# Optimization experiments

Hardware: AMD Instinct MI355X
Metric: run time of the kernel (lower is better)

The kernel has to match this reference:

```python
import jax, jax.numpy as jnp
import numpy as np

B, N, K, F_IN, F_OUT = 8, 2048, 32, 256, 256


def setup_inputs() -> dict:
    key = jax.random.key(0)
    ks = jax.random.split(key, 8)
    x = jax.random.normal(ks[0], (B, N, F_IN), dtype=jnp.float32)
    idx_neib = jax.random.randint(ks[1], (N, K), 0, N, dtype=jnp.int32)
    # Linear params (torch nn.Linear stores weight as [out, in])
    lim_x = np.sqrt(2.0) * np.sqrt(6.0 / (F_IN + F_OUT))  # xavier_uniform, gain=relu
    Wx_w = jax.random.uniform(ks[2], (F_OUT, F_IN), jnp.float32, -lim_x, lim_x)
    Wx_b = jnp.zeros((F_OUT,), jnp.float32)
    Wn_w = jax.random.uniform(ks[3], (F_OUT, F_IN), jnp.float32, -lim_x, lim_x)
    Wn_b = jnp.zeros((F_OUT,), jnp.float32)
    gamma = jnp.ones((2 * F_OUT,), jnp.float32)
    beta = jnp.zeros((2 * F_OUT,), jnp.float32)
    return {"x": x, "idx_neib": idx_neib, "Wx_w": Wx_w, "Wx_b": Wx_b,
            "Wn_w": Wn_w, "Wn_b": Wn_b, "gamma": gamma, "beta": beta}


def reference(x, idx_neib, Wx_w, Wx_b, Wn_w, Wn_b, gamma, beta):
    # Gather neighbor features: [B, N, K, F] then mean over the K neighbors.
    x_neib = jnp.take(x, idx_neib, axis=1).mean(axis=2)  # [B, N, F]
    # Dual linear projections (weights stored [out, in] as in torch).
    h_self = jnp.einsum('bnf,of->bno', x, Wx_w) + Wx_b
    h_nei = jnp.einsum('bnf,of->bno', x_neib, Wn_w) + Wn_b
    h = jnp.concatenate([h_self, h_nei], axis=2)          # [B, N, 2*out]
    # F.normalize(p=2, dim=2): divide by max(||h||_2, 1e-12)
    nrm = jnp.sqrt(jnp.sum(h * h, axis=2, keepdims=True))
    h = h / jnp.maximum(nrm, 1e-12)
    h = jax.nn.relu(h)
    # BatchNorm1d over channel dim (training mode: batch stats over B and N,
    # biased variance), eps=1e-5.
    mu = h.mean(axis=(0, 1))
    var = jnp.mean((h - mu) ** 2, axis=(0, 1))
    h = (h - mu) * jax.lax.rsqrt(var + 1e-5) * gamma + beta
    return h
```

## Files before the change

kernel.cpp:

```cpp
#include <hip/hip_runtime.h>
#include <stdint.h>

#define BB 8
#define NN 2048
#define KK 32
#define FIN 256
#define FOUT 256
#define CC 512
#define MM (BB*NN)
#define RB 32
#define NBLK (MM/RB)
#define LDA 264

typedef __attribute__((ext_vector_type(8))) short short8;
typedef __attribute__((ext_vector_type(4))) float f32x4;
typedef __attribute__((ext_vector_type(2))) float f32x2;

__device__ __forceinline__ unsigned short f2bf(float f) {
    union { float f; unsigned u; } v; v.f = f;
    unsigned u = v.u;
    return (unsigned short)((u + 0x7FFFu + ((u >> 16) & 1u)) >> 16);
}
__device__ __forceinline__ float bf2f(unsigned short s) {
    union { unsigned u; float f; } v; v.u = ((unsigned)s) << 16;
    return v.f;
}
__device__ __forceinline__ f32x2 bfpair(unsigned u) {
    union { unsigned u; float f; } lo, hi;
    lo.u = u << 16;
    hi.u = u & 0xFFFF0000u;
    return (f32x2){lo.f, hi.f};
}

__global__ void k_prep(const float* __restrict__ Wx, const float* __restrict__ Wxb,
                       const float* __restrict__ Wn, const float* __restrict__ Wnb,
                       const float* __restrict__ x,
                       unsigned short* __restrict__ Wc, float* __restrict__ bc,
                       unsigned short* __restrict__ xb,
                       float* __restrict__ psum8, unsigned* __restrict__ cnt) {
    const int blk = blockIdx.x;
    const int tid = threadIdx.x;
    if (blk < 128) {
        if (blk == 0) {
            float4 z = {0.f, 0.f, 0.f, 0.f};
            #pragma unroll
            for (int i = 0; i < (CC * 16 / 4) / 256; ++i)
                ((float4*)psum8)[tid + i * 256] = z;
            if (tid == 0) *cnt = 0u;
        }
        int gid = blk * 256 + tid;
        int e0 = gid * 4;
        int o = e0 >> 8, k = e0 & 255;
        const float* src = (o < FOUT) ? (Wx + o * FIN + k) : (Wn + (o - FOUT) * FIN + k);
        float4 v = *(const float4*)src;
        ushort4 p; p.x = f2bf(v.x); p.y = f2bf(v.y); p.z = f2bf(v.z); p.w = f2bf(v.w);
        *(ushort4*)(Wc + e0) = p;
        if (gid < 128) {
            int c0 = gid * 4;
            float4 bv = (c0 < FOUT) ? *(const float4*)(Wxb + c0)
                                    : *(const float4*)(Wnb + c0 - FOUT);
            *(float4*)(bc + c0) = bv;
        }
    } else {
        size_t gid = (size_t)(blk - 128) * 256 + tid;
        size_t e0 = gid * 8;
        float4 v0 = *(const float4*)(x + e0);
        float4 v1 = *(const float4*)(x + e0 + 4);
        ushort4 p0, p1;
        p0.x = f2bf(v0.x); p0.y = f2bf(v0.y); p0.z = f2bf(v0.z); p0.w = f2bf(v0.w);
        p1.x = f2bf(v1.x); p1.y = f2bf(v1.y); p1.z = f2bf(v1.z); p1.w = f2bf(v1.w);
        *(ushort4*)(xb + e0)     = p0;
        *(ushort4*)(xb + e0 + 4) = p1;
    }
}

__global__ __launch_bounds__(512, 4)
void k_gemm(const unsigned short* __restrict__ xb, const int* __restrict__ idx,
            const unsigned short* __restrict__ Wc,
            const float* __restrict__ bc,
            const float* __restrict__ gamma, const float* __restrict__ beta,
            unsigned short* __restrict__ h,
            float* __restrict__ psum8, float* __restrict__ psq8,
            float* __restrict__ ss, unsigned* __restrict__ cnt) {
    __shared__ unsigned short As[2][RB * LDA];
    __shared__ float sqpart[8][RB];
    __shared__ float rnorm[RB];
    __shared__ unsigned lastf;

    const int bid  = blockIdx.x;
    const int tid  = threadIdx.x;
    const int w    = tid >> 6;
    const int lane = tid & 63;
    const int quad = lane >> 4;
    const int l16  = lane & 15;
    const int p    = lane >> 5;
    const int l32  = lane & 31;
    const int b    = bid & 7;
    const int n0   = (bid >> 3) * RB;
    const unsigned short* xbat = xb + (size_t)b * NN * FIN;
    const size_t r0g = (size_t)b * NN + n0;

    {
        const uint4* gs = (const uint4*)(xbat + (size_t)n0 * FIN);
        #pragma unroll
        for (int i = 0; i < 2; ++i) {
            int e = tid + i * 512;
            *(uint4*)&As[0][(e >> 5) * LDA + (e & 31) * 8] = gs[e];
        }
    }
    {
        const int* ip = idx + (n0 + (w << 2)) * KK;
        const unsigned short* xp = xbat + l32 * 8;
        f32x2 ac[4][4];
        #pragma unroll
        for (int rr = 0; rr < 4; ++rr)
            #pragma unroll
            for (int c = 0; c < 4; ++c) ac[rr][c] = (f32x2){0.f, 0.f};

        #pragma unroll 4
        for (int k = 0; k < 16; ++k) {
            int kk = (k << 1) | p;
            int j0 = ip[0 * KK + kk];
            int j1 = ip[1 * KK + kk];
            int j2 = ip[2 * KK + kk];
            int j3 = ip[3 * KK + kk];
            uint4 v0 = *(const uint4*)(xp + (size_t)j0 * FIN);
            uint4 v1 = *(const uint4*)(xp + (size_t)j1 * FIN);
            uint4 v2 = *(const uint4*)(xp + (size_t)j2 * FIN);
            uint4 v3 = *(const uint4*)(xp + (size_t)j3 * FIN);
            const unsigned* u0 = (const unsigned*)&v0;
            const unsigned* u1 = (const unsigned*)&v1;
            const unsigned* u2 = (const unsigned*)&v2;
            const unsigned* u3 = (const unsigned*)&v3;
            #pragma unroll
            for (int c = 0; c < 4; ++c) {
                ac[0][c] += bfpair(u0[c]);
                ac[1][c] += bfpair(u1[c]);
                ac[2][c] += bfpair(u2[c]);
                ac[3][c] += bfpair(u3[c]);
            }
        }
        const float s = 1.0f / (float)KK;
        #pragma unroll
        for (int rr = 0; rr < 4; ++rr) {
            #pragma unroll
            for (int c = 0; c < 4; ++c) {
                ac[rr][c][0] += __shfl_xor(ac[rr][c][0], 32, 64);
                ac[rr][c][1] += __shfl_xor(ac[rr][c][1], 32, 64);
            }
            if (p == 0) {
                unsigned short o8[8];
                #pragma unroll
                for (int c = 0; c < 4; ++c) {
                    o8[2 * c]     = f2bf(ac[rr][c][0] * s);
                    o8[2 * c + 1] = f2bf(ac[rr][c][1] * s);
                }
                *(uint4*)&As[1][((w << 2) + rr) * LDA + l32 * 8] = *(const uint4*)o8;
            }
        }
    }
    __syncthreads();

    const int half = w >> 2;
    const unsigned short* A = As[half];
    const int cbg = half * 256 + (w & 3) * 64;

    f32x4 acc[2][4];
    #pragma unroll
    for (int mt = 0; mt < 2; ++mt)
        #pragma unroll
        for (int nt = 0; nt < 4; ++nt) acc[mt][nt] = (f32x4){0.f, 0.f, 0.f, 0.f};

    const unsigned short* Bp = Wc + (size_t)(cbg + l16) * FIN + quad * 8;
    const unsigned short* Ap = A + (size_t)l16 * LDA + quad * 8;

    #pragma unroll 2
    for (int k0 = 0; k0 < FIN; k0 += 32) {
        short8 a0 = *(const short8*)(Ap + k0);
        short8 a1 = *(const short8*)(Ap + 16 * LDA + k0);
        short8 bfr[4];
        #pragma unroll
        for (int nt = 0; nt < 4; ++nt)
            bfr[nt] = *(const short8*)(Bp + (size_t)nt * 16 * FIN + k0);
        #pragma unroll
        for (int nt = 0; nt < 4; ++nt) {
            acc[0][nt] = __builtin_amdgcn_mfma_f32_16x16x32_bf16(a0, bfr[nt], acc[0][nt], 0, 0, 0);
            acc[1][nt] = __builtin_amdgcn_mfma_f32_16x16x32_bf16(a1, bfr[nt], acc[1][nt], 0, 0, 0);
        }
    }

    float bcv[4];
    #pragma unroll
    for (int nt = 0; nt < 4; ++nt) bcv[nt] = bc[cbg + nt * 16 + l16];

    float rsq[2][4] = {{0.f,0.f,0.f,0.f},{0.f,0.f,0.f,0.f}};
    #pragma unroll
    for (int mt = 0; mt < 2; ++mt)
        #pragma unroll
        for (int nt = 0; nt < 4; ++nt)
            #pragma unroll
            for (int r = 0; r < 4; ++r) {
                float v = acc[mt][nt][r] + bcv[nt];
                acc[mt][nt][r] = v;
                rsq[mt][r] += v * v;
            }
    #pragma unroll
    for (int off = 1; off < 16; off <<= 1)
        #pragma unroll
        for (int mt = 0; mt < 2; ++mt)
            #pragma unroll
            for (int r = 0; r < 4; ++r)
                rsq[mt][r] += __shfl_xor(rsq[mt][r], off, 64);
    if (l16 == 0) {
        #pragma unroll
        for (int mt = 0; mt < 2; ++mt)
            #pragma unroll
            for (int r = 0; r < 4; ++r)
                sqpart[w][mt * 16 + quad * 4 + r] = rsq[mt][r];
    }
    __syncthreads();
    if (tid < RB) {
        float tot = 0.f;
        #pragma unroll
        for (int i = 0; i < 8; ++i) tot += sqpart[i][tid];
        rnorm[tid] = 1.0f / fmaxf(sqrtf(tot), 1e-12f);
    }
    __syncthreads();

    float csum[4] = {0.f,0.f,0.f,0.f};
    float csq [4] = {0.f,0.f,0.f,0.f};
    #pragma unroll
    for (int mt = 0; mt < 2; ++mt) {
        #pragma unroll
        for (int r = 0; r < 4; ++r) {
            int row = mt * 16 + quad * 4 + r;
            float rn = rnorm[row];
            unsigned short* hp = h + (r0g + row) * CC + cbg + l16;
            #pragma unroll
            for (int nt = 0; nt < 4; ++nt) {
                float v = fmaxf(acc[mt][nt][r] * rn, 0.0f);
                hp[nt * 16] = f2bf(v);
                csum[nt] += v;
                csq [nt] += v * v;
            }
        }
    }
    #pragma unroll
    for (int off = 16; off < 64; off <<= 1)
        #pragma unroll
        for (int nt = 0; nt < 4; ++nt) {
            csum[nt] += __shfl_xor(csum[nt], off, 64);
            csq [nt] += __shfl_xor(csq [nt], off, 64);
        }
    if (quad == 0) {
        #pragma unroll
        for (int nt = 0; nt < 4; ++nt) {
            int c = cbg + nt * 16 + l16;
            __hip_atomic_fetch_add(&psum8[c * 8 + b], csum[nt],
                                   __ATOMIC_RELAXED, __HIP_MEMORY_SCOPE_AGENT);
            __hip_atomic_fetch_add(&psq8[c * 8 + b], csq[nt],
                                   __ATOMIC_RELAXED, __HIP_MEMORY_SCOPE_AGENT);
        }
    }

    __syncthreads();
    if (tid == 0) {
        unsigned prev = __hip_atomic_fetch_add(cnt, 1u, __ATOMIC_ACQ_REL,
                                               __HIP_MEMORY_SCOPE_AGENT);
        lastf = (prev == (unsigned)(NBLK - 1)) ? 1u : 0u;
    }
    __syncthreads();
    if (lastf) {
        if (tid < CC) {
            float S = 0.f, Q = 0.f;
            #pragma unroll
            for (int i = 0; i < 8; ++i) {
                S += __hip_atomic_load(&psum8[tid * 8 + i], __ATOMIC_RELAXED,
                                       __HIP_MEMORY_SCOPE_AGENT);
                Q += __hip_atomic_load(&psq8[tid * 8 + i], __ATOMIC_RELAXED,
                                       __HIP_MEMORY_SCOPE_AGENT);
            }
            const float inv = 1.0f / (float)MM;
            float mu  = S * inv;
            float var = fmaxf(Q * inv - mu * mu, 0.0f);
            float sc  = gamma[tid] * rsqrtf(var + 1e-5f);
            ss[tid]      = sc;
            ss[CC + tid] = beta[tid] - mu * sc;
        }
    }
}

__global__ void k_apply(const unsigned short* __restrict__ h,
                        const float* __restrict__ ss,
                        float* __restrict__ out) {
    const int x   = blockIdx.x & 7;
    const int j   = blockIdx.x >> 3;
    const int tid = threadIdx.x;
    const size_t e0 = (size_t)x * ((size_t)NN * CC) + (size_t)j * 2048 + (size_t)tid * 8;
    int c0 = (int)(e0 & (CC - 1));
    uint4 hv = *(const uint4*)(h + e0);
    const unsigned short* hs = (const unsigned short*)&hv;
    float4 sc0 = *(const float4*)(ss + c0);
    float4 sc1 = *(const float4*)(ss + c0 + 4);
    float4 sh0 = *(const float4*)(ss + CC + c0);
    float4 sh1 = *(const float4*)(ss + CC + c0 + 4);
    float4 o0, o1;
    o0.x = bf2f(hs[0]) * sc0.x + sh0.x;
    o0.y = bf2f(hs[1]) * sc0.y + sh0.y;
    o0.z = bf2f(hs[2]) * sc0.z + sh0.z;
    o0.w = bf2f(hs[3]) * sc0.w + sh0.w;
    o1.x = bf2f(hs[4]) * sc1.x + sh1.x;
    o1.y = bf2f(hs[5]) * sc1.y + sh1.y;
    o1.z = bf2f(hs[6]) * sc1.z + sh1.z;
    o1.w = bf2f(hs[7]) * sc1.w + sh1.w;
    *(float4*)(out + e0)     = o0;
    *(float4*)(out + e0 + 4) = o1;
}

extern "C" void kernel_launch(void* const* d_in, const int* in_sizes, int n_in,
                              void* d_out, int out_size, void* d_ws, size_t ws_size,
                              hipStream_t stream) {
    const float* x     = (const float*)d_in[0];
    const int*   idx   = (const int*)  d_in[1];
    const float* Wx_w  = (const float*)d_in[2];
    const float* Wx_b  = (const float*)d_in[3];
    const float* Wn_w  = (const float*)d_in[4];
    const float* Wn_b  = (const float*)d_in[5];
    const float* gamma = (const float*)d_in[6];
    const float* beta  = (const float*)d_in[7];
    float* out = (float*)d_out;

    char* p = (char*)d_ws;
    unsigned short* xb = (unsigned short*)p; p += (size_t)MM * FIN * 2;
    unsigned short* Wc = (unsigned short*)p; p += (size_t)CC * FIN * 2;
    float* bc          = (float*)p;          p += (size_t)CC * 4;
    unsigned short* h  = (unsigned short*)p; p += (size_t)MM * CC * 2;
    float* psum8       = (float*)p;          p += (size_t)CC * 8 * 4;
    float* psq8        = (float*)p;          p += (size_t)CC * 8 * 4;
    float* ss          = (float*)p;          p += (size_t)2 * CC * 4;
    unsigned* cnt      = (unsigned*)p;       p += 64;

    hipLaunchKernelGGL(k_prep,  dim3(2176), dim3(256), 0, stream,
                       Wx_w, Wx_b, Wn_w, Wn_b, x, Wc, bc, xb, psum8, cnt);
    hipLaunchKernelGGL(k_gemm,  dim3(NBLK), dim3(512), 0, stream,
                       xb, idx, Wc, bc, gamma, beta, h, psum8, psq8, ss, cnt);
    hipLaunchKernelGGL(k_apply, dim3(4096), dim3(256), 0, stream, h, ss, out);
}
```

Measured before the change: 151.4 us.

## Move BatchNorm stat finalization into apply kernel, drop last-block counter

Removes the atomic last-block counter and serial finalization tail from the GEMM kernel. Each apply block now recomputes the per-channel scale and shift from the partial sums into padded shared memory. The partial-sum layout changes from channel-major to batch-major, and the gather loop unroll drops from 4 to 2. This trades a serialized tail and a global counter atomic for redundant small reductions in every apply block.

```diff
diff --git a/kernel.cpp b/kernel.cpp
--- a/kernel.cpp
+++ b/kernel.cpp
@@ -37,7 +37,7 @@
                        const float* __restrict__ x,
                        unsigned short* __restrict__ Wc, float* __restrict__ bc,
                        unsigned short* __restrict__ xb,
-                       float* __restrict__ psum8, unsigned* __restrict__ cnt) {
+                       float* __restrict__ psum8) {
     const int blk = blockIdx.x;
     const int tid = threadIdx.x;
     if (blk < 128) {
@@ -46,7 +46,6 @@
             #pragma unroll
             for (int i = 0; i < (CC * 16 / 4) / 256; ++i)
                 ((float4*)psum8)[tid + i * 256] = z;
-            if (tid == 0) *cnt = 0u;
         }
         int gid = blk * 256 + tid;
         int e0 = gid * 4;
@@ -78,14 +77,11 @@
 void k_gemm(const unsigned short* __restrict__ xb, const int* __restrict__ idx,
             const unsigned short* __restrict__ Wc,
             const float* __restrict__ bc,
-            const float* __restrict__ gamma, const float* __restrict__ beta,
             unsigned short* __restrict__ h,
-            float* __restrict__ psum8, float* __restrict__ psq8,
-            float* __restrict__ ss, unsigned* __restrict__ cnt) {
+            float* __restrict__ psum8, float* __restrict__ psq8) {
     __shared__ unsigned short As[2][RB * LDA];
     __shared__ float sqpart[8][RB];
     __shared__ float rnorm[RB];
-    __shared__ unsigned lastf;
 
     const int bid  = blockIdx.x;
     const int tid  = threadIdx.x;
@@ -117,7 +113,7 @@
             #pragma unroll
             for (int c = 0; c < 4; ++c) ac[rr][c] = (f32x2){0.f, 0.f};
 
-        #pragma unroll 4
+        #pragma unroll 2
         for (int k = 0; k < 16; ++k) {
             int kk = (k << 1) | p;
             int j0 = ip[0 * KK + kk];
@@ -256,63 +252,62 @@
         #pragma unroll
         for (int nt = 0; nt < 4; ++nt) {
             int c = cbg + nt * 16 + l16;
-            __hip_atomic_fetch_add(&psum8[c * 8 + b], csum[nt],
+            __hip_atomic_fetch_add(&psum8[b * CC + c], csum[nt],
                                    __ATOMIC_RELAXED, __HIP_MEMORY_SCOPE_AGENT);
-            __hip_atomic_fetch_add(&psq8[c * 8 + b], csq[nt],
+            __hip_atomic_fetch_add(&psq8[b * CC + c], csq[nt],
                                    __ATOMIC_RELAXED, __HIP_MEMORY_SCOPE_AGENT);
         }
     }
-
+}
+
+__global__ __launch_bounds__(256)
+void k_apply(const unsigned short* __restrict__ h,
+             const float* __restrict__ psum8, const float* __restrict__ psq8,
+             const float* __restrict__ gamma, const float* __restrict__ beta,
+             float* __restrict__ out) {
+    __shared__ float ssc[CC + (CC >> 3)];
+    __shared__ float ssh[CC + (CC >> 3)];
+    const int tid = threadIdx.x;
+    {
+        const int c = tid * 2;
+        float2 S = {0.f, 0.f}, Q = {0.f, 0.f};
+        #pragma unroll
+        for (int i = 0; i < 8; ++i) {
+            float2 a = *(const float2*)(psum8 + i * CC + c);
+            float2 b = *(const float2*)(psq8  + i * CC + c);
+            S.x += a.x; S.y += a.y; Q.x += b.x; Q.y += b.y;
+        }
+        const float inv = 1.0f / (float)MM;
+        float2 g  = *(const float2*)(gamma + c);
+        float2 be = *(const float2*)(beta + c);
+        float mu0 = S.x * inv, mu1 = S.y * inv;
+        float v0 = fmaxf(Q.x * inv - mu0 * mu0, 0.0f);
+        float v1 = fmaxf(Q.y * inv - mu1 * mu1, 0.0f);
+        float sc0 = g.x * rsqrtf(v0 + 1e-5f);
+        float sc1 = g.y * rsqrtf(v1 + 1e-5f);
+        int pc = c + (c >> 3);
+        ssc[pc]     = sc0; ssc[pc + 1] = sc1;
+        ssh[pc]     = be.x - mu0 * sc0;
+        ssh[pc + 1] = be.y - mu1 * sc1;
+    }
     __syncthreads();
-    if (tid == 0) {
-        unsigned prev = __hip_atomic_fetch_add(cnt, 1u, __ATOMIC_ACQ_REL,
-                                               __HIP_MEMORY_SCOPE_AGENT);
-        lastf = (prev == (unsigned)(NBLK - 1)) ? 1u : 0u;
-    }
-    __syncthreads();
-    if (lastf) {
-        if (tid < CC) {
-            float S = 0.f, Q = 0.f;
-            #pragma unroll
-            for (int i = 0; i < 8; ++i) {
-                S += __hip_atomic_load(&psum8[tid * 8 + i], __ATOMIC_RELAXED,
-                                       __HIP_MEMORY_SCOPE_AGENT);
-                Q += __hip_atomic_load(&psq8[tid * 8 + i], __ATOMIC_RELAXED,
-                                       __HIP_MEMORY_SCOPE_AGENT);
-            }
-            const float inv = 1.0f / (float)MM;
-            float mu  = S * inv;
-            float var = fmaxf(Q * inv - mu * mu, 0.0f);
-            float sc  = gamma[tid] * rsqrtf(var + 1e-5f);
-            ss[tid]      = sc;
-            ss[CC + tid] = beta[tid] - mu * sc;
-        }
-    }
-}
-
-__global__ void k_apply(const unsigned short* __restrict__ h,
-                        const float* __restrict__ ss,
-                        float* __restrict__ out) {
-    const int x   = blockIdx.x & 7;
-    const int j   = blockIdx.x >> 3;
-    const int tid = threadIdx.x;
+
+    const int x = blockIdx.x & 7;
+    const int j = blockIdx.x >> 3;
     const size_t e0 = (size_t)x * ((size_t)NN * CC) + (size_t)j * 2048 + (size_t)tid * 8;
-    int c0 = (int)(e0 & (CC - 1));
+    const int c0 = (int)(e0 & (CC - 1));
+    const int pb = c0 + (c0 >> 3);
     uint4 hv = *(const uint4*)(h + e0);
     const unsigned short* hs = (const unsigned short*)&hv;
-    float4 sc0 = *(const float4*)(ss + c0);
-    float4 sc1 = *(const float4*)(ss + c0 + 4);
-    float4 sh0 = *(const float4*)(ss + CC + c0);
-    float4 sh1 = *(const float4*)(ss + CC + c0 + 4);
     float4 o0, o1;
-    o0.x = bf2f(hs[0]) * sc0.x + sh0.x;
-    o0.y = bf2f(hs[1]) * sc0.y + sh0.y;
-    o0.z = bf2f(hs[2]) * sc0.z + sh0.z;
-    o0.w = bf2f(hs[3]) * sc0.w + sh0.w;
-    o1.x = bf2f(hs[4]) * sc1.x + sh1.x;
-    o1.y = bf2f(hs[5]) * sc1.y + sh1.y;
-    o1.z = bf2f(hs[6]) * sc1.z + sh1.z;
-    o1.w = bf2f(hs[7]) * sc1.w + sh1.w;
+    o0.x = bf2f(hs[0]) * ssc[pb + 0] + ssh[pb + 0];
+    o0.y = bf2f(hs[1]) * ssc[pb + 1] + ssh[pb + 1];
+    o0.z = bf2f(hs[2]) * ssc[pb + 2] + ssh[pb + 2];
+    o0.w = bf2f(hs[3]) * ssc[pb + 3] + ssh[pb + 3];
+    o1.x = bf2f(hs[4]) * ssc[pb + 4] + ssh[pb + 4];
+    o1.y = bf2f(hs[5]) * ssc[pb + 5] + ssh[pb + 5];
+    o1.z = bf2f(hs[6]) * ssc[pb + 6] + ssh[pb + 6];
+    o1.w = bf2f(hs[7]) * ssc[pb + 7] + ssh[pb + 7];
     *(float4*)(out + e0)     = o0;
     *(float4*)(out + e0 + 4) = o1;
 }
@@ -335,14 +330,13 @@
     unsigned short* Wc = (unsigned short*)p; p += (size_t)CC * FIN * 2;
     float* bc          = (float*)p;          p += (size_t)CC * 4;
     unsigned short* h  = (unsigned short*)p; p += (size_t)MM * CC * 2;
-    float* psum8       = (float*)p;          p += (size_t)CC * 8 * 4;
-    float* psq8        = (float*)p;          p += (size_t)CC * 8 * 4;
-    float* ss          = (float*)p;          p += (size_t)2 * CC * 4;
-    unsigned* cnt      = (unsigned*)p;       p += 64;
+    float* psum8       = (float*)p;          p += (size_t)8 * CC * 4;
+    float* psq8        = (float*)p;          p += (size_t)8 * CC * 4;
 
     hipLaunchKernelGGL(k_prep,  dim3(2176), dim3(256), 0, stream,
-                       Wx_w, Wx_b, Wn_w, Wn_b, x, Wc, bc, xb, psum8, cnt);
+                       Wx_w, Wx_b, Wn_w, Wn_b, x, Wc, bc, xb, psum8);
     hipLaunchKernelGGL(k_gemm,  dim3(NBLK), dim3(512), 0, stream,
-                       xb, idx, Wc, bc, gamma, beta, h, psum8, psq8, ss, cnt);
-    hipLaunchKernelGGL(k_apply, dim3(4096), dim3(256), 0, stream, h, ss, out);
-}
+                       xb, idx, Wc, bc, h, psum8, psq8);
+    hipLaunchKernelGGL(k_apply, dim3(4096), dim3(256), 0, stream,
+                       h, psum8, psq8, gamma, beta, out);
+}
```

After: 135.3 us. -10.7%, faster.
